# Optimization experiments

Hardware: AMD Instinct MI355X
Metric: run time of the kernel (lower is better)

The kernel has to match this reference:

```python
import jax, jax.numpy as jnp
import numpy as np

B, S, D = 4, 2048, 1024
P = 9            # num_paths
DM = D // 4      # bottleneck d_mid
EPS = 1e-5


def setup_inputs() -> dict:
    key = jax.random.key(0)
    ks = jax.random.split(key, 12)
    sc_in = 1.0 / np.sqrt(D)
    sc_mid = 1.0 / np.sqrt(DM)
    return {
        "x": jax.random.normal(ks[0], (B, S, D), dtype=jnp.float32),
        # neighbor mixer: per-channel 3-tap kernel over the sequence axis
        "mix_kernel": jax.random.normal(ks[1], (3, D), dtype=jnp.float32) * 0.5,
        # 9 parallel bottleneck paths: D -> D/4 -> D
        "W1": jax.random.normal(ks[2], (P, D, DM), dtype=jnp.float32) * sc_in,
        "b1": jnp.zeros((P, DM), dtype=jnp.float32),
        "W2": jax.random.normal(ks[3], (P, DM, D), dtype=jnp.float32) * sc_mid,
        "b2": jnp.zeros((P, D), dtype=jnp.float32),
        # observer: D -> D/4 -> tanh -> ... -> P scores
        "Wo1": jax.random.normal(ks[4], (D, DM), dtype=jnp.float32) * sc_in,
        "bo1": jnp.zeros((DM,), dtype=jnp.float32),
        "Wo2": jax.random.normal(ks[5], (DM, P), dtype=jnp.float32) * sc_mid,
        "bo2": jnp.zeros((P,), dtype=jnp.float32),
        # output norm affine params
        "gamma": jnp.ones((D,), dtype=jnp.float32),
        "beta": jnp.zeros((D,), dtype=jnp.float32),
    }


def _mix(x, mix_kernel):
    # eidosNeighborMixer: local 3-tap depthwise mix along sequence (non-causal)
    xp = jnp.pad(x, ((0, 0), (1, 1), (0, 0)))
    return (mix_kernel[0] * xp[:, :-2]
            + mix_kernel[1] * xp[:, 1:-1]
            + mix_kernel[2] * xp[:, 2:])


def _layernorm(h, gamma, beta):
    mu = jnp.mean(h, axis=-1, keepdims=True)
    var = jnp.var(h, axis=-1, keepdims=True)
    return (h - mu) * jax.lax.rsqrt(var + EPS) * gamma + beta


def reference(x, mix_kernel, W1, b1, W2, b2, Wo1, bo1, Wo2, bo2, gamma, beta):
    x_mixed = _mix(x, mix_kernel)                                   # [B,S,D]
    # all num_paths bottleneck transforms computed densely (as in source)
    h = jnp.einsum("bsd,pdm->bspm", x_mixed, W1) + b1               # [B,S,P,DM]
    stacked_paths = jnp.einsum("bspm,pmd->bspd", h, W2) + b2        # [B,S,P,D]
    # observer scores
    scores = jnp.tanh(x_mixed @ Wo1 + bo1) @ Wo2 + bo2              # [B,S,P]
    # eval-mode collapse: hard argmax one-hot selection
    idx = jnp.argmax(scores, axis=-1)                               # [B,S]
    weights = jax.nn.one_hot(idx, P, dtype=stacked_paths.dtype)     # [B,S,P]
    collapsed = jnp.einsum("bspd,bsp->bsd", stacked_paths, weights)  # [B,S,D]
    return _layernorm(x + collapsed, gamma, beta)
```

## Files before the change

kernel.cpp:

```cpp
#include <hip/hip_runtime.h>
#include <math.h>

#define Ss 2048
#define Dd 1024
#define Pp 9
#define DMm 256
#define Tt 8192
#define EPSf 1e-5f
#define BAND 6e-3f

typedef __attribute__((ext_vector_type(8))) __bf16 bf16x8;
typedef __attribute__((ext_vector_type(4))) float f32x4;

#define GLOBAL_AS __attribute__((address_space(1)))
#define LDS_AS __attribute__((address_space(3)))

#define MAXTILES 137

__device__ __forceinline__ unsigned short bf16rn(float f) {
  unsigned int u = __float_as_uint(f);
  unsigned int r = (u + 0x7fffu + ((u >> 16) & 1u)) >> 16;
  return (unsigned short)r;
}

__device__ __forceinline__ void gload16(const void* g, void* l) {
  __builtin_amdgcn_global_load_lds((const GLOBAL_AS unsigned int*)g,
                                   (LDS_AS unsigned int*)l, 16, 0, 0);
}

#define KSW(r, sl) (((r) << 6) + ((((sl) ^ ((r) & 7))) << 3))

__global__ __launch_bounds__(256) void k_mix2(const float* __restrict__ x,
    const float* __restrict__ mk, unsigned short* __restrict__ xh,
    int* __restrict__ counts) {
  if (blockIdx.x == 0 && threadIdx.x < 64) counts[threadIdx.x] = 0;
  const int t = blockIdx.x;
  const int s = t & (Ss - 1);
  const int d = threadIdx.x << 2;
  const float* xc = x + (size_t)t * Dd + d;
  float4 vb = *(const float4*)xc;
  float4 va = make_float4(0.f, 0.f, 0.f, 0.f);
  float4 vc = make_float4(0.f, 0.f, 0.f, 0.f);
  if (s > 0)      va = *(const float4*)(xc - Dd);
  if (s < Ss - 1) vc = *(const float4*)(xc + Dd);
  const float4 k0 = *(const float4*)(mk + d);
  const float4 k1 = *(const float4*)(mk + Dd + d);
  const float4 k2 = *(const float4*)(mk + 2 * Dd + d);
  float4 o;
  o.x = k0.x * va.x + k1.x * vb.x + k2.x * vc.x;
  o.y = k0.y * va.y + k1.y * vb.y + k2.y * vc.y;
  o.z = k0.z * va.z + k1.z * vb.z + k2.z * vc.z;
  o.w = k0.w * va.w + k1.w * vb.w + k2.w * vc.w;
  ushort4 h;
  h.x = bf16rn(o.x); h.y = bf16rn(o.y); h.z = bf16rn(o.z); h.w = bf16rn(o.w);
  *(ushort4*)(xh + (size_t)t * Dd + d) = h;
}

__global__ __launch_bounds__(256) void k_cvt_all(
    const float* __restrict__ W1, const float* __restrict__ W2,
    const float* __restrict__ Wo1,
    unsigned short* __restrict__ W1t, unsigned short* __restrict__ W2t,
    unsigned short* __restrict__ Wo1t) {
  const int z = blockIdx.z;
  const float* in; unsigned short* outp; int R, C, r0, c0;
  if (z < Pp)            { in = W1;  outp = W1t;  R = Dd;  C = DMm;
                           r0 = blockIdx.x * 32; c0 = blockIdx.y * 32; }
  else if (z < 2 * Pp)   { in = W2;  outp = W2t;  R = DMm; C = Dd;
                           r0 = blockIdx.y * 32; c0 = blockIdx.x * 32; }
  else                   { in = Wo1; outp = Wo1t; R = Dd;  C = DMm;
                           r0 = blockIdx.x * 32; c0 = blockIdx.y * 32; }
  const int zi = (z < Pp) ? z : ((z < 2 * Pp) ? z - Pp : 0);
  const size_t zo = (size_t)zi * R * C;
  __shared__ float tile[32][33];
  const int tr = threadIdx.x >> 3, tc = (threadIdx.x & 7) << 2;
  float4 v = *(const float4*)(in + zo + (size_t)(r0 + tr) * C + c0 + tc);
  tile[tr][tc] = v.x; tile[tr][tc + 1] = v.y; tile[tr][tc + 2] = v.z; tile[tr][tc + 3] = v.w;
  __syncthreads();
  ushort4 h;
  h.x = bf16rn(tile[tc + 0][tr]); h.y = bf16rn(tile[tc + 1][tr]);
  h.z = bf16rn(tile[tc + 2][tr]); h.w = bf16rn(tile[tc + 3][tr]);
  *(ushort4*)(outp + zo + (size_t)(c0 + tr) * R + r0 + tc) = h;
}

template<int KTOT, int NTOT, int MODE, bool GROUPED>
__global__ __launch_bounds__(256) void k_gemm(
    const unsigned short* __restrict__ A,
    const unsigned short* __restrict__ Bt,
    const float* __restrict__ bias,
    const float* __restrict__ resid,
    float* __restrict__ outf, unsigned short* __restrict__ outh,
    const int* __restrict__ counts, const int* __restrict__ tokenlist) {
  int p = 0, ti = blockIdx.x, cnt = Tt;
  if (GROUPED) {
    for (p = 0; p < Pp; ++p) {
      cnt = counts[p];
      const int nt = (cnt + 63) >> 6;
      if (ti < nt) break;
      ti -= nt;
    }
    if (p == Pp) return;
  }
  const int tile0 = ti * 64;
  __shared__ int tl[64];
  __shared__ __align__(16) unsigned short As[2][64 * 64];
  __shared__ __align__(16) unsigned short Bs[2][128 * 64];
  const int tid = threadIdx.x;
  if (tid < 64) {
    const int li = tile0 + tid;
    if (GROUPED) tl[tid] = (li < cnt) ? tokenlist[p * Tt + li] : tokenlist[p * Tt];
    else         tl[tid] = li;
  }
  __syncthreads();
  const int w = tid >> 6, lane = tid & 63;
  const int fr = lane & 15, fs = lane >> 4;
  const int wr = w >> 1, wc = w & 1;
  const int n0 = blockIdx.y * 128;
  const unsigned short* Bp0 = Bt + (size_t)p * NTOT * KTOT + (size_t)n0 * KTOT;
  const unsigned short* srcA[2];
  #pragma unroll
  for (int i = 0; i < 2; ++i) {
    const int u = i * 256 + tid, r = u >> 3, sl = (u & 7) ^ (r & 7);
    srcA[i] = A + (size_t)tl[r] * KTOT + sl * 8;
  }
  const unsigned short* srcB[4];
  #pragma unroll
  for (int i = 0; i < 4; ++i) {
    const int u = i * 256 + tid, r = u >> 3, sl = (u & 7) ^ (r & 7);
    srcB[i] = Bp0 + (size_t)r * KTOT + sl * 8;
  }
  const int ldsW = w * 512;
  int aoff[2][2], boff[4][2];
  #pragma unroll
  for (int m = 0; m < 2; ++m)
    #pragma unroll
    for (int kk = 0; kk < 2; ++kk)
      aoff[m][kk] = KSW(wr * 32 + m * 16 + fr, kk * 4 + fs);
  #pragma unroll
  for (int n = 0; n < 4; ++n)
    #pragma unroll
    for (int kk = 0; kk < 2; ++kk)
      boff[n][kk] = KSW(wc * 64 + n * 16 + fr, kk * 4 + fs);

#define STAGE(b, kb) do { \
    gload16(srcA[0] + (kb), &As[b][0] + ldsW); \
    gload16(srcA[1] + (kb), &As[b][0] + 2048 + ldsW); \
    gload16(srcB[0] + (kb), &Bs[b][0] + ldsW); \
    gload16(srcB[1] + (kb), &Bs[b][0] + 2048 + ldsW); \
    gload16(srcB[2] + (kb), &Bs[b][0] + 4096 + ldsW); \
    gload16(srcB[3] + (kb), &Bs[b][0] + 6144 + ldsW); \
  } while (0)

  f32x4 acc[2][4] = {};
  const int NS = KTOT / 64;
  STAGE(0, 0);
  for (int s = 0; s < NS; ++s) {
    const int buf = s & 1;
    if (s + 1 < NS) {
      STAGE(buf ^ 1, (s + 1) * 64);
      asm volatile("s_waitcnt vmcnt(6)" ::: "memory");
    } else {
      asm volatile("s_waitcnt vmcnt(0)" ::: "memory");
    }
    __builtin_amdgcn_s_barrier();
    __builtin_amdgcn_sched_barrier(0);
    const unsigned short* Ab = &As[buf][0];
    const unsigned short* Bb_ = &Bs[buf][0];
    bf16x8 a[2][2], b[4][2];
    #pragma unroll
    for (int m = 0; m < 2; ++m)
      #pragma unroll
      for (int kk = 0; kk < 2; ++kk)
        a[m][kk] = *(const bf16x8*)&Ab[aoff[m][kk]];
    #pragma unroll
    for (int n = 0; n < 4; ++n)
      #pragma unroll
      for (int kk = 0; kk < 2; ++kk)
        b[n][kk] = *(const bf16x8*)&Bb_[boff[n][kk]];
    #pragma unroll
    for (int kk = 0; kk < 2; ++kk)
      #pragma unroll
      for (int m = 0; m < 2; ++m)
        #pragma unroll
        for (int n = 0; n < 4; ++n)
          acc[m][n] = __builtin_amdgcn_mfma_f32_16x16x32_bf16(a[m][kk], b[n][kk], acc[m][n], 0, 0, 0);
    __builtin_amdgcn_s_barrier();
  }
#undef STAGE

  const float* bias_z = bias + (size_t)p * NTOT;
  #pragma unroll
  for (int m = 0; m < 2; ++m) {
    #pragma unroll
    for (int j = 0; j < 4; ++j) {
      const int rr = wr * 32 + m * 16 + fs * 4 + j;
      const int li = tile0 + rr;
      if (GROUPED && li >= cnt) continue;
      const int t = tl[rr];
      #pragma unroll
      for (int n = 0; n < 4; ++n) {
        const int c = n0 + wc * 64 + n * 16 + fr;
        const float v = acc[m][n][j] + bias_z[c];
        if (MODE == 0)      outf[(size_t)t * NTOT + c] = tanhf(v);
        else if (MODE == 1) outh[(size_t)t * NTOT + c] = bf16rn(v);
        else                outf[(size_t)t * NTOT + c] = v + resid[(size_t)t * NTOT + c];
      }
    }
  }
}

__global__ __launch_bounds__(256) void k_score(const float* __restrict__ hidden,
    const float* __restrict__ Wo2, const float* __restrict__ bo2,
    int* __restrict__ idx, int* __restrict__ nflag, int* __restrict__ flagged) {
  __shared__ float sW[DMm * Pp];
  const int tid = threadIdx.x;
  for (int l = tid; l < DMm * Pp; l += 256) sW[l] = Wo2[l];
  __syncthreads();
  const int wave = tid >> 6, lane = tid & 63;
  const int t = blockIdx.x * 4 + wave;
  const float4 h = *(const float4*)(hidden + (size_t)t * DMm + lane * 4);
  const int m = lane * 4;
  float part[Pp];
  #pragma unroll
  for (int pp = 0; pp < Pp; ++pp)
    part[pp] = h.x * sW[(m + 0) * Pp + pp] + h.y * sW[(m + 1) * Pp + pp]
             + h.z * sW[(m + 2) * Pp + pp] + h.w * sW[(m + 3) * Pp + pp];
  #pragma unroll
  for (int off = 32; off > 0; off >>= 1)
    #pragma unroll
    for (int pp = 0; pp < Pp; ++pp)
      part[pp] += __shfl_xor(part[pp], off);
  if (lane == 0) {
    float best = -1e30f, second = -1e30f;
    int bi = 0;
    #pragma unroll
    for (int pp = 0; pp < Pp; ++pp) {
      const float sc = part[pp] + bo2[pp];
      if (sc > best) { second = best; best = sc; bi = pp; }
      else if (sc > second) second = sc;
    }
    idx[t] = bi;
    if (best - second < BAND) {
      const int pos = atomicAdd(nflag, 1);
      flagged[pos] = t;
    }
  }
}

__global__ __launch_bounds__(256) void k_rescue(const float* __restrict__ x,
    const float* __restrict__ mk,
    const float* __restrict__ Wo1, const float* __restrict__ bo1,
    const float* __restrict__ Wo2, const float* __restrict__ bo2,
    const int* __restrict__ nflag, const int* __restrict__ flagged,
    int* __restrict__ idx) {
  __shared__ double sx[Dd];
  __shared__ double th[DMm];
  __shared__ double red[4][12];
  const int nf = *nflag;
  const int tid = threadIdx.x;
  const int wv = tid >> 6, ln = tid & 63;
  for (int f = blockIdx.x; f < nf; f += gridDim.x) {
    const int t = flagged[f];
    const int s = t & (Ss - 1);
    for (int l = tid; l < Dd; l += 256) {
      const double xa = (s > 0)      ? (double)x[(size_t)(t - 1) * Dd + l] : 0.0;
      const double xb =                (double)x[(size_t)t * Dd + l];
      const double xc = (s < Ss - 1) ? (double)x[(size_t)(t + 1) * Dd + l] : 0.0;
      sx[l] = (double)mk[l] * xa + (double)mk[Dd + l] * xb + (double)mk[2 * Dd + l] * xc;
    }
    __syncthreads();
    {
      double a0 = 0, a1 = 0, a2 = 0, a3 = 0;
      const float* wcol = Wo1 + tid;
      for (int d = 0; d < Dd; d += 4) {
        a0 += sx[d + 0] * (double)wcol[(size_t)(d + 0) * DMm];
        a1 += sx[d + 1] * (double)wcol[(size_t)(d + 1) * DMm];
        a2 += sx[d + 2] * (double)wcol[(size_t)(d + 2) * DMm];
        a3 += sx[d + 3] * (double)wcol[(size_t)(d + 3) * DMm];
      }
      th[tid] = tanh(((a0 + a1) + (a2 + a3)) + (double)bo1[tid]);
    }
    __syncthreads();
    double pr[Pp];
    const double tv = th[tid];
    #pragma unroll
    for (int p = 0; p < Pp; ++p) pr[p] = tv * (double)Wo2[tid * Pp + p];
    #pragma unroll
    for (int off = 32; off > 0; off >>= 1)
      #pragma unroll
      for (int p = 0; p < Pp; ++p) pr[p] += __shfl_xor(pr[p], off);
    if (ln == 0) {
      #pragma unroll
      for (int p = 0; p < Pp; ++p) red[wv][p] = pr[p];
    }
    __syncthreads();
    if (tid == 0) {
      double best = -1e300; int bi = 0;
      #pragma unroll
      for (int p = 0; p < Pp; ++p) {
        const double sv = red[0][p] + red[1][p] + red[2][p] + red[3][p] + (double)bo2[p];
        if (sv > best) { best = sv; bi = p; }
      }
      idx[t] = bi;
    }
    __syncthreads();
  }
}

__global__ __launch_bounds__(256) void k_scatter(const int* __restrict__ idx,
    int* __restrict__ counts, int* __restrict__ tokenlist) {
  __shared__ int lcnt[Pp], lbase[Pp];
  const int tid = threadIdx.x;
  if (tid < Pp) lcnt[tid] = 0;
  __syncthreads();
  const int t = blockIdx.x * 256 + tid;
  const int p = idx[t];
  const int slot = atomicAdd(&lcnt[p], 1);
  __syncthreads();
  if (tid < Pp) lbase[tid] = atomicAdd(&counts[tid], lcnt[tid]);
  __syncthreads();
  tokenlist[p * Tt + lbase[p] + slot] = t;
}

__global__ __launch_bounds__(256) void k_ln(float* __restrict__ y,
    const float* __restrict__ gamma, const float* __restrict__ beta) {
  const int t = blockIdx.x;
  const int d = threadIdx.x << 2;
  float* row = y + (size_t)t * Dd;
  float4 v = *(float4*)(row + d);
  float s = v.x + v.y + v.z + v.w;
  float q = v.x * v.x + v.y * v.y + v.z * v.z + v.w * v.w;
  #pragma unroll
  for (int off = 32; off > 0; off >>= 1) {
    s += __shfl_xor(s, off);
    q += __shfl_xor(q, off);
  }
  __shared__ float ssum[4], sqq[4];
  const int wave = threadIdx.x >> 6, lane = threadIdx.x & 63;
  if (lane == 0) { ssum[wave] = s; sqq[wave] = q; }
  __syncthreads();
  s = ssum[0] + ssum[1] + ssum[2] + ssum[3];
  q = sqq[0] + sqq[1] + sqq[2] + sqq[3];
  const float mu = s * (1.f / Dd);
  const float var = q * (1.f / Dd) - mu * mu;
  const float inv = rsqrtf(var + EPSf);
  const float4 g = *(const float4*)(gamma + d);
  const float4 bt = *(const float4*)(beta + d);
  float4 o;
  o.x = (v.x - mu) * inv * g.x + bt.x;
  o.y = (v.y - mu) * inv * g.y + bt.y;
  o.z = (v.z - mu) * inv * g.z + bt.z;
  o.w = (v.w - mu) * inv * g.w + bt.w;
  *(float4*)(row + d) = o;
}

extern "C" void kernel_launch(void* const* d_in, const int* in_sizes, int n_in,
                              void* d_out, int out_size, void* d_ws, size_t ws_size,
                              hipStream_t stream) {
  (void)in_sizes; (void)n_in; (void)out_size; (void)ws_size;
  const float* x     = (const float*)d_in[0];
  const float* mk    = (const float*)d_in[1];
  const float* W1    = (const float*)d_in[2];
  const float* b1    = (const float*)d_in[3];
  const float* W2    = (const float*)d_in[4];
  const float* b2    = (const float*)d_in[5];
  const float* Wo1   = (const float*)d_in[6];
  const float* bo1   = (const float*)d_in[7];
  const float* Wo2   = (const float*)d_in[8];
  const float* bo2   = (const float*)d_in[9];
  const float* gamma = (const float*)d_in[10];
  const float* beta  = (const float*)d_in[11];
  float* out = (float*)d_out;

  size_t off = 0;
  auto alloc = [&](size_t bytes) -> void* {
    void* p = (char*)d_ws + off;
    off += (bytes + 255) & ~(size_t)255;
    return p;
  };
  unsigned short* xm_h   = (unsigned short*)alloc((size_t)Tt * Dd * 2);
  float*          hidden = (float*)alloc((size_t)Tt * DMm * 4);
  unsigned short* h1     = (unsigned short*)hidden;
  unsigned short* W1t    = (unsigned short*)alloc((size_t)Pp * Dd * DMm * 2);
  unsigned short* W2t    = (unsigned short*)alloc((size_t)Pp * DMm * Dd * 2);
  unsigned short* Wo1t   = (unsigned short*)alloc((size_t)Dd * DMm * 2);
  int* idx      = (int*)alloc(Tt * 4);
  int* counts   = (int*)alloc(64 * 4);
  int* nflag    = counts + 16;
  int* flagged  = (int*)alloc(Tt * 4);
  int* tokenlist = (int*)alloc((size_t)Pp * Tt * 4);

  k_mix2<<<Tt, 256, 0, stream>>>(x, mk, xm_h, counts);
  k_cvt_all<<<dim3(32, 8, 2 * Pp + 1), 256, 0, stream>>>(W1, W2, Wo1, W1t, W2t, Wo1t);

  k_gemm<Dd, DMm, 0, false><<<dim3(Tt / 64, DMm / 128), 256, 0, stream>>>(
      xm_h, Wo1t, bo1, nullptr, hidden, nullptr, nullptr, nullptr);
  k_score<<<Tt / 4, 256, 0, stream>>>(hidden, Wo2, bo2, idx, nflag, flagged);
  k_rescue<<<256, 256, 0, stream>>>(x, mk, Wo1, bo1, Wo2, bo2, nflag, flagged, idx);
  k_scatter<<<Tt / 256, 256, 0, stream>>>(idx, counts, tokenlist);

  k_gemm<Dd, DMm, 1, true><<<dim3(MAXTILES, DMm / 128), 256, 0, stream>>>(
      xm_h, W1t, b1, nullptr, nullptr, h1, counts, tokenlist);
  k_gemm<DMm, Dd, 2, true><<<dim3(MAXTILES, Dd / 128), 256, 0, stream>>>(
      h1, W2t, b2, x, out, nullptr, counts, tokenlist);
  k_ln<<<Tt, 256, 0, stream>>>(out, gamma, beta);
}
```

Before: 146.7 us.

## Merge prep kernels, fold scatter into scoring, shrink GEMM M-tile to 32

Combines the mix and weight-conversion kernels into one launch. The token-bucketing scatter moves into the score kernel, and the rescue kernel appends its flagged tokens directly, which removes two launches. The GEMM row tile drops from 64 to 32 so more blocks run and the grouped GEMMs waste fewer padded rows. In exchange each block does less reuse of the B tile, the score kernel now loops over 16 tokens per wave, and the order of entries in the token lists changes.

```diff
diff --git a/kernel.cpp b/kernel.cpp
--- a/kernel.cpp
+++ b/kernel.cpp
@@ -15,7 +15,7 @@
 #define GLOBAL_AS __attribute__((address_space(1)))
 #define LDS_AS __attribute__((address_space(3)))
 
-#define MAXTILES 137
+#define MAXT32 (Tt / 32 + Pp)
 
 __device__ __forceinline__ unsigned short bf16rn(float f) {
   unsigned int u = __float_as_uint(f);
@@ -30,45 +30,44 @@
 
 #define KSW(r, sl) (((r) << 6) + ((((sl) ^ ((r) & 7))) << 3))
 
-__global__ __launch_bounds__(256) void k_mix2(const float* __restrict__ x,
+__global__ __launch_bounds__(256) void k_prep(const float* __restrict__ x,
     const float* __restrict__ mk, unsigned short* __restrict__ xh,
-    int* __restrict__ counts) {
-  if (blockIdx.x == 0 && threadIdx.x < 64) counts[threadIdx.x] = 0;
-  const int t = blockIdx.x;
-  const int s = t & (Ss - 1);
-  const int d = threadIdx.x << 2;
-  const float* xc = x + (size_t)t * Dd + d;
-  float4 vb = *(const float4*)xc;
-  float4 va = make_float4(0.f, 0.f, 0.f, 0.f);
-  float4 vc = make_float4(0.f, 0.f, 0.f, 0.f);
-  if (s > 0)      va = *(const float4*)(xc - Dd);
-  if (s < Ss - 1) vc = *(const float4*)(xc + Dd);
-  const float4 k0 = *(const float4*)(mk + d);
-  const float4 k1 = *(const float4*)(mk + Dd + d);
-  const float4 k2 = *(const float4*)(mk + 2 * Dd + d);
-  float4 o;
-  o.x = k0.x * va.x + k1.x * vb.x + k2.x * vc.x;
-  o.y = k0.y * va.y + k1.y * vb.y + k2.y * vc.y;
-  o.z = k0.z * va.z + k1.z * vb.z + k2.z * vc.z;
-  o.w = k0.w * va.w + k1.w * vb.w + k2.w * vc.w;
-  ushort4 h;
-  h.x = bf16rn(o.x); h.y = bf16rn(o.y); h.z = bf16rn(o.z); h.w = bf16rn(o.w);
-  *(ushort4*)(xh + (size_t)t * Dd + d) = h;
-}
-
-__global__ __launch_bounds__(256) void k_cvt_all(
     const float* __restrict__ W1, const float* __restrict__ W2,
     const float* __restrict__ Wo1,
     unsigned short* __restrict__ W1t, unsigned short* __restrict__ W2t,
-    unsigned short* __restrict__ Wo1t) {
-  const int z = blockIdx.z;
+    unsigned short* __restrict__ Wo1t, int* __restrict__ counts) {
+  const int bid = blockIdx.x;
+  if (bid < Tt) {
+    if (bid == 0 && threadIdx.x < 64) counts[threadIdx.x] = 0;
+    const int t = bid;
+    const int s = t & (Ss - 1);
+    const int d = threadIdx.x << 2;
+    const float* xc = x + (size_t)t * Dd + d;
+    float4 vb = *(const float4*)xc;
+    float4 va = make_float4(0.f, 0.f, 0.f, 0.f);
+    float4 vc = make_float4(0.f, 0.f, 0.f, 0.f);
+    if (s > 0)      va = *(const float4*)(xc - Dd);
+    if (s < Ss - 1) vc = *(const float4*)(xc + Dd);
+    const float4 k0 = *(const float4*)(mk + d);
+    const float4 k1 = *(const float4*)(mk + Dd + d);
+    const float4 k2 = *(const float4*)(mk + 2 * Dd + d);
+    float4 o;
+    o.x = k0.x * va.x + k1.x * vb.x + k2.x * vc.x;
+    o.y = k0.y * va.y + k1.y * vb.y + k2.y * vc.y;
+    o.z = k0.z * va.z + k1.z * vb.z + k2.z * vc.z;
+    o.w = k0.w * va.w + k1.w * vb.w + k2.w * vc.w;
+    ushort4 h;
+    h.x = bf16rn(o.x); h.y = bf16rn(o.y); h.z = bf16rn(o.z); h.w = bf16rn(o.w);
+    *(ushort4*)(xh + (size_t)t * Dd + d) = h;
+    return;
+  }
+  const int i = bid - Tt;
+  const int z = i >> 8, rem = i & 255;
+  const int bx = rem & 31, by = rem >> 5;
   const float* in; unsigned short* outp; int R, C, r0, c0;
-  if (z < Pp)            { in = W1;  outp = W1t;  R = Dd;  C = DMm;
-                           r0 = blockIdx.x * 32; c0 = blockIdx.y * 32; }
-  else if (z < 2 * Pp)   { in = W2;  outp = W2t;  R = DMm; C = Dd;
-                           r0 = blockIdx.y * 32; c0 = blockIdx.x * 32; }
-  else                   { in = Wo1; outp = Wo1t; R = Dd;  C = DMm;
-                           r0 = blockIdx.x * 32; c0 = blockIdx.y * 32; }
+  if (z < Pp)          { in = W1;  outp = W1t;  R = Dd;  C = DMm; r0 = bx * 32; c0 = by * 32; }
+  else if (z < 2 * Pp) { in = W2;  outp = W2t;  R = DMm; C = Dd;  r0 = by * 32; c0 = bx * 32; }
+  else                 { in = Wo1; outp = Wo1t; R = Dd;  C = DMm; r0 = bx * 32; c0 = by * 32; }
   const int zi = (z < Pp) ? z : ((z < 2 * Pp) ? z - Pp : 0);
   const size_t zo = (size_t)zi * R * C;
   __shared__ float tile[32][33];
@@ -94,18 +93,18 @@
   if (GROUPED) {
     for (p = 0; p < Pp; ++p) {
       cnt = counts[p];
-      const int nt = (cnt + 63) >> 6;
+      const int nt = (cnt + 31) >> 5;
       if (ti < nt) break;
       ti -= nt;
     }
     if (p == Pp) return;
   }
-  const int tile0 = ti * 64;
-  __shared__ int tl[64];
-  __shared__ __align__(16) unsigned short As[2][64 * 64];
+  const int tile0 = ti * 32;
+  __shared__ int tl[32];
+  __shared__ __align__(16) unsigned short As[2][32 * 64];
   __shared__ __align__(16) unsigned short Bs[2][128 * 64];
   const int tid = threadIdx.x;
-  if (tid < 64) {
+  if (tid < 32) {
     const int li = tile0 + tid;
     if (GROUPED) tl[tid] = (li < cnt) ? tokenlist[p * Tt + li] : tokenlist[p * Tt];
     else         tl[tid] = li;
@@ -116,12 +115,8 @@
   const int wr = w >> 1, wc = w & 1;
   const int n0 = blockIdx.y * 128;
   const unsigned short* Bp0 = Bt + (size_t)p * NTOT * KTOT + (size_t)n0 * KTOT;
-  const unsigned short* srcA[2];
-  #pragma unroll
-  for (int i = 0; i < 2; ++i) {
-    const int u = i * 256 + tid, r = u >> 3, sl = (u & 7) ^ (r & 7);
-    srcA[i] = A + (size_t)tl[r] * KTOT + sl * 8;
-  }
+  const int ua = tid, ra = ua >> 3, sa = (ua & 7) ^ (ra & 7);
+  const unsigned short* srcA = A + (size_t)tl[ra] * KTOT + sa * 8;
   const unsigned short* srcB[4];
   #pragma unroll
   for (int i = 0; i < 4; ++i) {
@@ -129,12 +124,9 @@
     srcB[i] = Bp0 + (size_t)r * KTOT + sl * 8;
   }
   const int ldsW = w * 512;
-  int aoff[2][2], boff[4][2];
-  #pragma unroll
-  for (int m = 0; m < 2; ++m)
-    #pragma unroll
-    for (int kk = 0; kk < 2; ++kk)
-      aoff[m][kk] = KSW(wr * 32 + m * 16 + fr, kk * 4 + fs);
+  int aoff[2], boff[4][2];
+  #pragma unroll
+  for (int kk = 0; kk < 2; ++kk) aoff[kk] = KSW(wr * 16 + fr, kk * 4 + fs);
   #pragma unroll
   for (int n = 0; n < 4; ++n)
     #pragma unroll
@@ -142,22 +134,21 @@
       boff[n][kk] = KSW(wc * 64 + n * 16 + fr, kk * 4 + fs);
 
 #define STAGE(b, kb) do { \
-    gload16(srcA[0] + (kb), &As[b][0] + ldsW); \
-    gload16(srcA[1] + (kb), &As[b][0] + 2048 + ldsW); \
+    gload16(srcA + (kb), &As[b][0] + ldsW); \
     gload16(srcB[0] + (kb), &Bs[b][0] + ldsW); \
     gload16(srcB[1] + (kb), &Bs[b][0] + 2048 + ldsW); \
     gload16(srcB[2] + (kb), &Bs[b][0] + 4096 + ldsW); \
     gload16(srcB[3] + (kb), &Bs[b][0] + 6144 + ldsW); \
   } while (0)
 
-  f32x4 acc[2][4] = {};
+  f32x4 acc[4] = {};
   const int NS = KTOT / 64;
   STAGE(0, 0);
   for (int s = 0; s < NS; ++s) {
     const int buf = s & 1;
     if (s + 1 < NS) {
       STAGE(buf ^ 1, (s + 1) * 64);
-      asm volatile("s_waitcnt vmcnt(6)" ::: "memory");
+      asm volatile("s_waitcnt vmcnt(5)" ::: "memory");
     } else {
       asm volatile("s_waitcnt vmcnt(0)" ::: "memory");
     }
@@ -165,12 +156,9 @@
     __builtin_amdgcn_sched_barrier(0);
     const unsigned short* Ab = &As[buf][0];
     const unsigned short* Bb_ = &Bs[buf][0];
-    bf16x8 a[2][2], b[4][2];
-    #pragma unroll
-    for (int m = 0; m < 2; ++m)
-      #pragma unroll
-      for (int kk = 0; kk < 2; ++kk)
-        a[m][kk] = *(const bf16x8*)&Ab[aoff[m][kk]];
+    bf16x8 a[2], b[4][2];
+    #pragma unroll
+    for (int kk = 0; kk < 2; ++kk) a[kk] = *(const bf16x8*)&Ab[aoff[kk]];
     #pragma unroll
     for (int n = 0; n < 4; ++n)
       #pragma unroll
@@ -179,71 +167,84 @@
     #pragma unroll
     for (int kk = 0; kk < 2; ++kk)
       #pragma unroll
-      for (int m = 0; m < 2; ++m)
-        #pragma unroll
-        for (int n = 0; n < 4; ++n)
-          acc[m][n] = __builtin_amdgcn_mfma_f32_16x16x32_bf16(a[m][kk], b[n][kk], acc[m][n], 0, 0, 0);
+      for (int n = 0; n < 4; ++n)
+        acc[n] = __builtin_amdgcn_mfma_f32_16x16x32_bf16(a[kk], b[n][kk], acc[n], 0, 0, 0);
     __builtin_amdgcn_s_barrier();
   }
 #undef STAGE
 
   const float* bias_z = bias + (size_t)p * NTOT;
   #pragma unroll
-  for (int m = 0; m < 2; ++m) {
-    #pragma unroll
-    for (int j = 0; j < 4; ++j) {
-      const int rr = wr * 32 + m * 16 + fs * 4 + j;
-      const int li = tile0 + rr;
-      if (GROUPED && li >= cnt) continue;
-      const int t = tl[rr];
-      #pragma unroll
-      for (int n = 0; n < 4; ++n) {
-        const int c = n0 + wc * 64 + n * 16 + fr;
-        const float v = acc[m][n][j] + bias_z[c];
-        if (MODE == 0)      outf[(size_t)t * NTOT + c] = tanhf(v);
-        else if (MODE == 1) outh[(size_t)t * NTOT + c] = bf16rn(v);
-        else                outf[(size_t)t * NTOT + c] = v + resid[(size_t)t * NTOT + c];
-      }
+  for (int j = 0; j < 4; ++j) {
+    const int rr = wr * 16 + fs * 4 + j;
+    const int li = tile0 + rr;
+    if (GROUPED && li >= cnt) continue;
+    const int t = tl[rr];
+    #pragma unroll
+    for (int n = 0; n < 4; ++n) {
+      const int c = n0 + wc * 64 + n * 16 + fr;
+      const float v = acc[n][j] + bias_z[c];
+      if (MODE == 0)      outf[(size_t)t * NTOT + c] = tanhf(v);
+      else if (MODE == 1) outh[(size_t)t * NTOT + c] = bf16rn(v);
+      else                outf[(size_t)t * NTOT + c] = v + resid[(size_t)t * NTOT + c];
     }
   }
 }
 
 __global__ __launch_bounds__(256) void k_score(const float* __restrict__ hidden,
     const float* __restrict__ Wo2, const float* __restrict__ bo2,
-    int* __restrict__ idx, int* __restrict__ nflag, int* __restrict__ flagged) {
+    int* __restrict__ idx, int* __restrict__ nflag, int* __restrict__ flagged,
+    int* __restrict__ counts, int* __restrict__ tokenlist) {
   __shared__ float sW[DMm * Pp];
+  __shared__ int lcnt[Pp], lbase[Pp];
   const int tid = threadIdx.x;
   for (int l = tid; l < DMm * Pp; l += 256) sW[l] = Wo2[l];
+  if (tid < Pp) lcnt[tid] = 0;
   __syncthreads();
   const int wave = tid >> 6, lane = tid & 63;
-  const int t = blockIdx.x * 4 + wave;
-  const float4 h = *(const float4*)(hidden + (size_t)t * DMm + lane * 4);
-  const int m = lane * 4;
-  float part[Pp];
-  #pragma unroll
-  for (int pp = 0; pp < Pp; ++pp)
-    part[pp] = h.x * sW[(m + 0) * Pp + pp] + h.y * sW[(m + 1) * Pp + pp]
-             + h.z * sW[(m + 2) * Pp + pp] + h.w * sW[(m + 3) * Pp + pp];
-  #pragma unroll
-  for (int off = 32; off > 0; off >>= 1)
+  int tArr[16], pArr[16], sArr[16];
+  #pragma unroll
+  for (int it = 0; it < 16; ++it) {
+    const int t = blockIdx.x * 64 + it * 4 + wave;
+    const float4 h = *(const float4*)(hidden + (size_t)t * DMm + lane * 4);
+    const int m = lane * 4;
+    float part[Pp];
     #pragma unroll
     for (int pp = 0; pp < Pp; ++pp)
-      part[pp] += __shfl_xor(part[pp], off);
-  if (lane == 0) {
-    float best = -1e30f, second = -1e30f;
-    int bi = 0;
-    #pragma unroll
-    for (int pp = 0; pp < Pp; ++pp) {
-      const float sc = part[pp] + bo2[pp];
-      if (sc > best) { second = best; best = sc; bi = pp; }
-      else if (sc > second) second = sc;
-    }
-    idx[t] = bi;
-    if (best - second < BAND) {
-      const int pos = atomicAdd(nflag, 1);
-      flagged[pos] = t;
-    }
-  }
+      part[pp] = h.x * sW[(m + 0) * Pp + pp] + h.y * sW[(m + 1) * Pp + pp]
+               + h.z * sW[(m + 2) * Pp + pp] + h.w * sW[(m + 3) * Pp + pp];
+    #pragma unroll
+    for (int off = 32; off > 0; off >>= 1)
+      #pragma unroll
+      for (int pp = 0; pp < Pp; ++pp)
+        part[pp] += __shfl_xor(part[pp], off);
+    tArr[it] = -1;
+    if (lane == 0) {
+      float best = -1e30f, second = -1e30f;
+      int bi = 0;
+      #pragma unroll
+      for (int pp = 0; pp < Pp; ++pp) {
+        const float sc = part[pp] + bo2[pp];
+        if (sc > best) { second = best; best = sc; bi = pp; }
+        else if (sc > second) second = sc;
+      }
+      idx[t] = bi;
+      if (best - second < BAND) {
+        const int pos = atomicAdd(nflag, 1);
+        flagged[pos] = t;
+      } else {
+        tArr[it] = t; pArr[it] = bi;
+        sArr[it] = atomicAdd(&lcnt[bi], 1);
+      }
+    }
+  }
+  __syncthreads();
+  if (tid < Pp) lbase[tid] = atomicAdd(&counts[tid], lcnt[tid]);
+  __syncthreads();
+  #pragma unroll
+  for (int it = 0; it < 16; ++it)
+    if (tArr[it] >= 0)
+      tokenlist[pArr[it] * Tt + lbase[pArr[it]] + sArr[it]] = tArr[it];
 }
 
 __global__ __launch_bounds__(256) void k_rescue(const float* __restrict__ x,
@@ -251,7 +252,7 @@
     const float* __restrict__ Wo1, const float* __restrict__ bo1,
     const float* __restrict__ Wo2, const float* __restrict__ bo2,
     const int* __restrict__ nflag, const int* __restrict__ flagged,
-    int* __restrict__ idx) {
+    int* __restrict__ idx, int* __restrict__ counts, int* __restrict__ tokenlist) {
   __shared__ double sx[Dd];
   __shared__ double th[DMm];
   __shared__ double red[4][12];
@@ -301,24 +302,11 @@
         if (sv > best) { best = sv; bi = p; }
       }
       idx[t] = bi;
+      const int pos = atomicAdd(&counts[bi], 1);
+      tokenlist[bi * Tt + pos] = t;
     }
     __syncthreads();
   }
-}
-
-__global__ __launch_bounds__(256) void k_scatter(const int* __restrict__ idx,
-    int* __restrict__ counts, int* __restrict__ tokenlist) {
-  __shared__ int lcnt[Pp], lbase[Pp];
-  const int tid = threadIdx.x;
-  if (tid < Pp) lcnt[tid] = 0;
-  __syncthreads();
-  const int t = blockIdx.x * 256 + tid;
-  const int p = idx[t];
-  const int slot = atomicAdd(&lcnt[p], 1);
-  __syncthreads();
-  if (tid < Pp) lbase[tid] = atomicAdd(&counts[tid], lcnt[tid]);
-  __syncthreads();
-  tokenlist[p * Tt + lbase[p] + slot] = t;
 }
 
 __global__ __launch_bounds__(256) void k_ln(float* __restrict__ y,
@@ -389,18 +377,19 @@
   int* flagged  = (int*)alloc(Tt * 4);
   int* tokenlist = (int*)alloc((size_t)Pp * Tt * 4);
 
-  k_mix2<<<Tt, 256, 0, stream>>>(x, mk, xm_h, counts);
-  k_cvt_all<<<dim3(32, 8, 2 * Pp + 1), 256, 0, stream>>>(W1, W2, Wo1, W1t, W2t, Wo1t);
-
-  k_gemm<Dd, DMm, 0, false><<<dim3(Tt / 64, DMm / 128), 256, 0, stream>>>(
+  k_prep<<<Tt + (2 * Pp + 1) * 256, 256, 0, stream>>>(
+      x, mk, xm_h, W1, W2, Wo1, W1t, W2t, Wo1t, counts);
+
+  k_gemm<Dd, DMm, 0, false><<<dim3(Tt / 32, DMm / 128), 256, 0, stream>>>(
       xm_h, Wo1t, bo1, nullptr, hidden, nullptr, nullptr, nullptr);
-  k_score<<<Tt / 4, 256, 0, stream>>>(hidden, Wo2, bo2, idx, nflag, flagged);
-  k_rescue<<<256, 256, 0, stream>>>(x, mk, Wo1, bo1, Wo2, bo2, nflag, flagged, idx);
-  k_scatter<<<Tt / 256, 256, 0, stream>>>(idx, counts, tokenlist);
-
-  k_gemm<Dd, DMm, 1, true><<<dim3(MAXTILES, DMm / 128), 256, 0, stream>>>(
+  k_score<<<Tt / 64, 256, 0, stream>>>(hidden, Wo2, bo2, idx, nflag, flagged,
+                                       counts, tokenlist);
+  k_rescue<<<256, 256, 0, stream>>>(x, mk, Wo1, bo1, Wo2, bo2, nflag, flagged,
+                                    idx, counts, tokenlist);
+
+  k_gemm<Dd, DMm, 1, true><<<dim3(MAXT32, DMm / 128), 256, 0, stream>>>(
       xm_h, W1t, b1, nullptr, nullptr, h1, counts, tokenlist);
-  k_gemm<DMm, Dd, 2, true><<<dim3(MAXTILES, Dd / 128), 256, 0, stream>>>(
+  k_gemm<DMm, Dd, 2, true><<<dim3(MAXT32, Dd / 128), 256, 0, stream>>>(
       h1, W2t, b2, x, out, nullptr, counts, tokenlist);
   k_ln<<<Tt, 256, 0, stream>>>(out, gamma, beta);
 }
```

After: 163.2 us. +11.3%, slower.
